# Kernel optimization log

Measured on AMD Instinct MI355X. Metric: run time of the kernel, lower is better.

The kernel has to match this reference:

```python
import jax, jax.numpy as jnp
import numpy as np

D_MODEL = 768
NHEAD = 12
HEAD_DIM = D_MODEL // NHEAD


def setup_inputs() -> dict:
    key = jax.random.key(0)
    ks = jax.random.split(key, 9)
    B, S = 1, 4096
    scale = 1.0 / np.sqrt(D_MODEL)
    x = jax.random.normal(ks[0], (B, S, D_MODEL), dtype=jnp.float32)
    # Linear params: weight [out,in] torch convention, bias [out]
    wq = jax.random.normal(ks[1], (D_MODEL, D_MODEL), dtype=jnp.float32) * scale
    bq = jnp.zeros((D_MODEL,), dtype=jnp.float32)
    wk = jax.random.normal(ks[2], (D_MODEL, D_MODEL), dtype=jnp.float32) * scale
    bk = jnp.zeros((D_MODEL,), dtype=jnp.float32)
    wv = jax.random.normal(ks[3], (D_MODEL, D_MODEL), dtype=jnp.float32) * scale
    bv = jnp.zeros((D_MODEL,), dtype=jnp.float32)
    wo = jax.random.normal(ks[4], (D_MODEL, D_MODEL), dtype=jnp.float32) * scale
    bo = jnp.zeros((D_MODEL,), dtype=jnp.float32)
    return {"x": x, "wq": wq, "bq": bq, "wk": wk, "bk": bk,
            "wv": wv, "bv": bv, "wo": wo, "bo": bo}


def reference(x, wq, bq, wk, bk, wv, bv, wo, bo):
    B, S, D = x.shape
    H, Hd = NHEAD, HEAD_DIM
    # projections (torch Linear: x @ W^T + b)
    q = (x @ wq.T + bq).reshape(B, S, H, Hd).transpose(0, 2, 1, 3)  # [B,H,S,Hd]
    k = (x @ wk.T + bk).reshape(B, S, H, Hd).transpose(0, 2, 1, 3)
    v = (x @ wv.T + bv).reshape(B, S, H, Hd).transpose(0, 2, 1, 3)
    scores = jnp.einsum('bhsd,bhtd->bhst', q, k) / jnp.sqrt(jnp.float32(Hd))  # [B,H,S,S]
    probs = jax.nn.softmax(scores, axis=-1)
    attn = jnp.einsum('bhst,bhtd->bhsd', probs, v)  # [B,H,S,Hd]
    attn = attn.transpose(0, 2, 1, 3).reshape(B, S, D)
    return attn @ wo.T + bo
```

## Files before the change

### kernel.cpp

```cpp
#include <hip/hip_runtime.h>
#include <hip/hip_bf16.h>

typedef __attribute__((ext_vector_type(8))) __bf16 bf16x8;
typedef __attribute__((ext_vector_type(4))) __bf16 bf16x4;
typedef __attribute__((ext_vector_type(4))) float f32x4;
typedef __attribute__((ext_vector_type(16))) float f32x16;
typedef __attribute__((ext_vector_type(2))) unsigned u32x2;

#define D_MODEL 768
#define SEQ     4096
#define NH      12
#define HD      64

#define QSCALE (0.125f * 1.44269504088896f)

__device__ __forceinline__ void gload_lds16(const void* g, void* l) {
    __builtin_amdgcn_global_load_lds(
        (const __attribute__((address_space(1))) void*)g,
        (__attribute__((address_space(3))) void*)l, 16, 0, 0);
}

__device__ __forceinline__ u32x2 plswap(unsigned a, unsigned b) {
    return __builtin_amdgcn_permlane32_swap(a, b, false, false);
}

__global__ __launch_bounds__(256) void cvt_kernel(
    const float* __restrict__ x,  const float* __restrict__ wq,
    const float* __restrict__ wk, const float* __restrict__ wv,
    const float* __restrict__ wo,
    __bf16* __restrict__ xb,  __bf16* __restrict__ wqb,
    __bf16* __restrict__ wkb, __bf16* __restrict__ wvb,
    __bf16* __restrict__ wob)
{
    const int XV = SEQ * D_MODEL / 4;
    const int WV = D_MODEL * D_MODEL / 4;
    const int total = XV + 4 * WV;
    for (int i = blockIdx.x * blockDim.x + threadIdx.x; i < total;
         i += gridDim.x * blockDim.x) {
        const float* src; __bf16* dst; int j;
        if      (i < XV)          { src = x;  dst = xb;  j = i; }
        else if (i < XV + WV)     { src = wq; dst = wqb; j = i - XV; }
        else if (i < XV + 2*WV)   { src = wk; dst = wkb; j = i - XV - WV; }
        else if (i < XV + 3*WV)   { src = wv; dst = wvb; j = i - XV - 2*WV; }
        else                      { src = wo; dst = wob; j = i - XV - 3*WV; }
        float4 v = ((const float4*)src)[j];
        bf16x4 o;
        o[0] = (__bf16)v.x; o[1] = (__bf16)v.y;
        o[2] = (__bf16)v.z; o[3] = (__bf16)v.w;
        ((bf16x4*)dst)[j] = o;
    }
}

__device__ __forceinline__ void gemm128_core(
    const __bf16* __restrict__ A, const __bf16* __restrict__ B, int KD,
    f32x4 acc[4][4], __bf16 (*As)[64], __bf16 (*Bs)[64])
{
    const int t = threadIdx.x;
    const int lane = t & 63, wid = t >> 6;
    const int wm = (wid & 1) * 64, wn = (wid >> 1) * 64;
    const int lr = lane & 15, lc = lane >> 4;
    const int rl = lane >> 3;
    const int cs = (lane & 7) ^ rl;

    const __bf16* ag = A + (size_t)(wid * 32 + rl) * KD + cs * 8;
    const __bf16* bg = B + (size_t)(wid * 32 + rl) * KD + cs * 8;

    for (int kt = 0; kt < KD / 64; ++kt) {
        __syncthreads();
        #pragma unroll
        for (int i = 0; i < 4; ++i) {
            gload_lds16(ag + (size_t)i * 8 * KD + kt * 64,
                        &As[wid * 32 + i * 8][0]);
            gload_lds16(bg + (size_t)i * 8 * KD + kt * 64,
                        &Bs[wid * 32 + i * 8][0]);
        }
        __syncthreads();

        #pragma unroll
        for (int kh = 0; kh < 2; ++kh) {
            bf16x8 af[4], bfr[4];
            #pragma unroll
            for (int mi = 0; mi < 4; ++mi)
                af[mi] = *(const bf16x8*)
                    &As[wm + mi * 16 + lr][(((kh << 2) | lc) ^ (lr & 7)) * 8];
            #pragma unroll
            for (int ni = 0; ni < 4; ++ni)
                bfr[ni] = *(const bf16x8*)
                    &Bs[wn + ni * 16 + lr][(((kh << 2) | lc) ^ (lr & 7)) * 8];
            __builtin_amdgcn_s_setprio(1);
            #pragma unroll
            for (int mi = 0; mi < 4; ++mi)
                #pragma unroll
                for (int ni = 0; ni < 4; ++ni)
                    acc[mi][ni] = __builtin_amdgcn_mfma_f32_16x16x32_bf16(
                        af[mi], bfr[ni], acc[mi][ni], 0, 0, 0);
            __builtin_amdgcn_s_setprio(0);
        }
    }
}

__global__ __launch_bounds__(256) void qkv_gemm(
    const __bf16* __restrict__ xb,
    const __bf16* __restrict__ wqb, const __bf16* __restrict__ wkb,
    const __bf16* __restrict__ wvb,
    const float* __restrict__ bq, const float* __restrict__ bk,
    const float* __restrict__ bv,
    __bf16* __restrict__ Qo, __bf16* __restrict__ Ko,
    __bf16* __restrict__ Vto)
{
    __shared__ __bf16 As[128][64];
    __shared__ __bf16 Bs[128][64];
    const int bm = blockIdx.x;
    const int seg = blockIdx.y / 6, bn = blockIdx.y % 6;
    const __bf16* B  = (seg == 0) ? wqb : (seg == 1) ? wkb : wvb;
    const float* bias = (seg == 0) ? bq : (seg == 1) ? bk : bv;

    f32x4 acc[4][4] = {};
    gemm128_core(xb + (size_t)bm * 128 * D_MODEL,
                 B  + (size_t)bn * 128 * D_MODEL, D_MODEL, acc, As, Bs);

    const int t = threadIdx.x, lane = t & 63, wid = t >> 6;
    const int wm = (wid & 1) * 64, wn = (wid >> 1) * 64;
    const int lr = lane & 15, lc = lane >> 4;
    const int m0 = bm * 128 + wm, n0 = bn * 128 + wn;

    if (seg < 2) {
        __bf16* O = (seg == 0) ? Qo : Ko;
        const float sc = (seg == 0) ? QSCALE : 1.0f;
        #pragma unroll
        for (int mi = 0; mi < 4; ++mi)
            #pragma unroll
            for (int ni = 0; ni < 4; ++ni) {
                int col = n0 + ni * 16 + lr;
                float bb = bias[col];
                #pragma unroll
                for (int r = 0; r < 4; ++r)
                    O[(size_t)(m0 + mi * 16 + lc * 4 + r) * D_MODEL + col] =
                        (__bf16)((acc[mi][ni][r] + bb) * sc);
            }
    } else {
        #pragma unroll
        for (int mi = 0; mi < 4; ++mi)
            #pragma unroll
            for (int ni = 0; ni < 4; ++ni) {
                int col = n0 + ni * 16 + lr;
                float bb = bias[col];
                bf16x4 pk;
                #pragma unroll
                for (int r = 0; r < 4; ++r)
                    pk[r] = (__bf16)(acc[mi][ni][r] + bb);
                *(bf16x4*)&Vto[(size_t)col * SEQ + m0 + mi * 16 + lc * 4] = pk;
            }
    }
}

__global__ __launch_bounds__(256) void attn_kernel(
    const __bf16* __restrict__ Q, const __bf16* __restrict__ K,
    const __bf16* __restrict__ Vt, __bf16* __restrict__ Attn)
{
    __shared__ __align__(16) char LDSc[32768];
    __bf16 (*Ks)[32][64] = (__bf16(*)[32][64])(LDSc);
    __bf16 (*Vs)[64][32] = (__bf16(*)[64][32])(LDSc + 16384);
    float* Mg = (float*)LDSc;
    float* Ml = (float*)(LDSc + 16384);

    const int bid = blockIdx.x;
    const int swz = (bid & 7) * 96 + (bid >> 3);
    const int h  = swz >> 6;
    const int q0 = (swz & 63) * 64;

    const int t = threadIdx.x, lane = t & 63, wid = t >> 6;
    const int qs = wid & 1, half = wid >> 1;
    const int ql = lane & 31, hi = lane >> 5;
    const int s7 = ql & 7;
    const int v2s = (ql >> 1) & 3;

    const int krl = lane >> 3, kcs = (lane & 7) ^ (lane >> 3);
    const int vrl = lane >> 2, vcs = (lane & 3) ^ ((lane >> 3) & 3);
    const __bf16* kg = K +
        (size_t)(half * 2048 + qs * 16 + krl) * D_MODEL + h * HD + kcs * 8;
    const __bf16* vg = Vt +
        (size_t)(h * HD + qs * 32 + vrl) * SEQ + half * 2048 + vcs * 8;

    const __bf16* qrow = Q + (size_t)(q0 + qs * 32 + ql) * D_MODEL + h * HD;
    bf16x8 qf[4];
    #pragma unroll
    for (int k4 = 0; k4 < 4; ++k4)
        qf[k4] = *(const bf16x8*)&qrow[k4 * 16 + hi * 8];

    f32x16 acc0 = {}, acc1 = {};
    float m_r = -1e30f, l_r = 0.f;

    gload_lds16(kg,                    &Ks[half * 2][qs * 16][0]);
    gload_lds16(kg + 8 * D_MODEL,      &Ks[half * 2][qs * 16 + 8][0]);
    gload_lds16(vg,                    &Vs[half * 2][qs * 32][0]);
    gload_lds16(vg + (size_t)16 * SEQ, &Vs[half * 2][qs * 32 + 16][0]);

    const int NT = 2048 / 32;

#define ATILE(CUR, PT, DOPF) do {                                             \
    __syncthreads();                                                          \
    if (DOPF) {                                                               \
        const __bf16* kgt = kg + (size_t)(PT) * 32 * D_MODEL;                 \
        const __bf16* vgt = vg + (PT) * 32;                                   \
        gload_lds16(kgt,               &Ks[half*2 + ((CUR)^1)][qs*16][0]);    \
        gload_lds16(kgt + 8*D_MODEL,   &Ks[half*2 + ((CUR)^1)][qs*16+8][0]);  \
        gload_lds16(vgt,               &Vs[half*2 + ((CUR)^1)][qs*32][0]);    \
        gload_lds16(vgt + (size_t)16*SEQ,                                     \
                    &Vs[half*2 + ((CUR)^1)][qs*32+16][0]);                    \
    }                                                                         \
    f32x16 st = {};                                                           \
    __builtin_amdgcn_s_setprio(1);                                            \
    _Pragma("unroll")                                                         \
    for (int k4 = 0; k4 < 4; ++k4) {                                          \
        bf16x8 kf = *(const bf16x8*)                                          \
            &Ks[half*2 + (CUR)][ql][((k4*2 + hi) ^ s7) * 8];                  \
        st = __builtin_amdgcn_mfma_f32_32x32x16_bf16(kf, qf[k4], st, 0,0,0);  \
    }                                                                         \
    __builtin_amdgcn_s_setprio(0);                                            \
    float mx = -1e30f;                                                        \
    _Pragma("unroll")                                                         \
    for (int r = 0; r < 16; ++r) mx = fmaxf(mx, st[r]);                       \
    {                                                                         \
        u32x2 mp = plswap(__float_as_uint(mx), __float_as_uint(mx));          \
        mx = fmaxf(__uint_as_float(mp[0]), __uint_as_float(mp[1]));           \
    }                                                                         \
    const bool skip = (bool)__all(mx - m_r <= 8.0f);                          \
    float mnew = skip ? m_r : fmaxf(m_r, mx);                                 \
    float corr = skip ? 1.0f : exp2f(m_r - mnew);                             \
    float rs = 0.f;                                                           \
    _Pragma("unroll")                                                         \
    for (int r = 0; r < 16; ++r) { st[r] = exp2f(st[r] - mnew); rs += st[r]; }\
    {                                                                         \
        u32x2 rp = plswap(__float_as_uint(rs), __float_as_uint(rs));          \
        rs = __uint_as_float(rp[0]) + __uint_as_float(rp[1]);                 \
    }                                                                         \
    l_r = l_r * corr + rs;  m_r = mnew;                                       \
    if (!skip) {                                                              \
        _Pragma("unroll")                                                     \
        for (int r = 0; r < 16; ++r) { acc0[r] *= corr; acc1[r] *= corr; }    \
    }                                                                         \
                                             \
    unsigned wA[4], wB[4];                                                    \
    _Pragma("unroll")                                                         \
    for (int g = 0; g < 4; ++g) {                                             \
        union { __bf16 h2[2]; unsigned u; } pa, pb;                           \
        pa.h2[0] = (__bf16)st[4*g + 0]; pa.h2[1] = (__bf16)st[4*g + 1];       \
        pb.h2[0] = (__bf16)st[4*g + 2]; pb.h2[1] = (__bf16)st[4*g + 3];       \
        wA[g] = pa.u; wB[g] = pb.u;                                           \
    }                                                                         \
    __builtin_amdgcn_s_setprio(1);                                            \
    _Pragma("unroll")                                                         \
    for (int kb = 0; kb < 2; ++kb) {                                          \
        u32x2 sA = plswap(wA[2*kb], wA[2*kb + 1]);                            \
        u32x2 sB = plswap(wB[2*kb], wB[2*kb + 1]);                            \
        union { unsigned u[4]; bf16x8 v; } fb;                                \
        fb.u[0] = sA[0]; fb.u[1] = sB[0]; fb.u[2] = sA[1]; fb.u[3] = sB[1];   \
        bf16x8 vf0 = *(const bf16x8*)                                         \
            &Vs[half*2 + (CUR)][ql][((kb*2 + hi) ^ v2s) * 8];                 \
        bf16x8 vf1 = *(const bf16x8*)                                         \
            &Vs[half*2 + (CUR)][32 + ql][((kb*2 + hi) ^ v2s) * 8];            \
        acc0 = __builtin_amdgcn_mfma_f32_32x32x16_bf16(vf0, fb.v, acc0,0,0,0);\
        acc1 = __builtin_amdgcn_mfma_f32_32x32x16_bf16(vf1, fb.v, acc1,0,0,0);\
    }                                                                         \
    __builtin_amdgcn_s_setprio(0);                                            \
} while (0)

    for (int kk = 0; kk < NT; kk += 2) {
        ATILE(0, kk + 1, 1);
        ATILE(1, kk + 2, (kk + 2 < NT));
    }
#undef ATILE

    __syncthreads();
    if (half == 1) {
        float* mybuf = Mg + qs * 2048 + lane * 32;
        #pragma unroll
        for (int j = 0; j < 4; ++j) {
            f32x4 v; v[0]=acc0[4*j]; v[1]=acc0[4*j+1]; v[2]=acc0[4*j+2]; v[3]=acc0[4*j+3];
            *(f32x4*)&mybuf[(j ^ s7) * 4] = v;
        }
        #pragma unroll
        for (int j = 0; j < 4; ++j) {
            f32x4 v; v[0]=acc1[4*j]; v[1]=acc1[4*j+1]; v[2]=acc1[4*j+2]; v[3]=acc1[4*j+3];
            *(f32x4*)&mybuf[((4 + j) ^ s7) * 4] = v;
        }
        Ml[(qs * 2 + 0) * 64 + lane] = m_r;
        Ml[(qs * 2 + 1) * 64 + lane] = l_r;
    }
    __syncthreads();
    if (half == 0) {
        float m1 = Ml[(qs * 2 + 0) * 64 + lane];
        float l1 = Ml[(qs * 2 + 1) * 64 + lane];
        float mstar = fmaxf(m_r, m1);
        float s0 = exp2f(m_r - mstar), s1 = exp2f(m1 - mstar);
        float li = 1.0f / (l_r * s0 + l1 * s1);
        const float* obuf = Mg + qs * 2048 + lane * 32;

        __bf16* orow = Attn + (size_t)(q0 + qs * 32 + ql) * D_MODEL
                       + h * HD + hi * 4;
        #pragma unroll
        for (int g = 0; g < 4; ++g) {
            f32x4 a1 = *(const f32x4*)&obuf[(g ^ s7) * 4];
            union { __bf16 h4[4]; uint2 v2; } w;
            #pragma unroll
            for (int i = 0; i < 4; ++i)
                w.h4[i] = (__bf16)((acc0[4*g+i] * s0 + a1[i] * s1) * li);
            *(uint2*)&orow[g * 8] = w.v2;

            f32x4 b1 = *(const f32x4*)&obuf[((4 + g) ^ s7) * 4];
            #pragma unroll
            for (int i = 0; i < 4; ++i)
                w.h4[i] = (__bf16)((acc1[4*g+i] * s0 + b1[i] * s1) * li);
            *(uint2*)&orow[32 + g * 8] = w.v2;
        }
    }
}

__global__ __launch_bounds__(256) void out_gemm(
    const __bf16* __restrict__ Ab, const __bf16* __restrict__ wob,
    const float* __restrict__ bo, float* __restrict__ out)
{
    __shared__ __bf16 As[128][64];
    __shared__ __bf16 Bs[128][64];
    const int bm = blockIdx.x, bn = blockIdx.y;
    f32x4 acc[4][4] = {};
    gemm128_core(Ab  + (size_t)bm * 128 * D_MODEL,
                 wob + (size_t)bn * 128 * D_MODEL, D_MODEL, acc, As, Bs);

    const int t = threadIdx.x, lane = t & 63, wid = t >> 6;
    const int wm = (wid & 1) * 64, wn = (wid >> 1) * 64;
    const int lr = lane & 15, lc = lane >> 4;
    const int m0 = bm * 128 + wm, n0 = bn * 128 + wn;
    #pragma unroll
    for (int mi = 0; mi < 4; ++mi)
        #pragma unroll
        for (int ni = 0; ni < 4; ++ni) {
            int col = n0 + ni * 16 + lr;
            float bb = bo[col];
            #pragma unroll
            for (int r = 0; r < 4; ++r)
                out[(size_t)(m0 + mi * 16 + lc * 4 + r) * D_MODEL + col] =
                    acc[mi][ni][r] + bb;
        }
}

extern "C" void kernel_launch(void* const* d_in, const int* in_sizes, int n_in,
                              void* d_out, int out_size, void* d_ws, size_t ws_size,
                              hipStream_t stream) {
    const float* x  = (const float*)d_in[0];
    const float* wq = (const float*)d_in[1];
    const float* bq = (const float*)d_in[2];
    const float* wk = (const float*)d_in[3];
    const float* bk = (const float*)d_in[4];
    const float* wv = (const float*)d_in[5];
    const float* bv = (const float*)d_in[6];
    const float* wo = (const float*)d_in[7];
    const float* bo = (const float*)d_in[8];

    char* ws = (char*)d_ws;
    const size_t XB_SZ = (size_t)SEQ * D_MODEL * 2;
    const size_t W_SZ  = (size_t)D_MODEL * D_MODEL * 2;
    __bf16* xb  = (__bf16*)(ws);
    __bf16* wqb = (__bf16*)(ws + XB_SZ);
    __bf16* wkb = (__bf16*)(ws + XB_SZ + W_SZ);
    __bf16* wvb = (__bf16*)(ws + XB_SZ + 2 * W_SZ);
    __bf16* wob = (__bf16*)(ws + XB_SZ + 3 * W_SZ);
    __bf16* Qb  = (__bf16*)(ws + XB_SZ + 4 * W_SZ);
    __bf16* Kb  = (__bf16*)(ws + 2 * XB_SZ + 4 * W_SZ);
    __bf16* Vtb = (__bf16*)(ws + 3 * XB_SZ + 4 * W_SZ);
    __bf16* Ab  = (__bf16*)(ws + 4 * XB_SZ + 4 * W_SZ);

    cvt_kernel<<<1024, 256, 0, stream>>>(x, wq, wk, wv, wo,
                                         xb, wqb, wkb, wvb, wob);
    qkv_gemm<<<dim3(32, 18), 256, 0, stream>>>(xb, wqb, wkb, wvb,
                                               bq, bk, bv, Qb, Kb, Vtb);
    attn_kernel<<<768, 256, 0, stream>>>(Qb, Kb, Vtb, Ab);
    out_gemm<<<dim3(32, 6), 256, 0, stream>>>(Ab, wob, bo, (float*)d_out);
}
```

Before: 162.9 us.

## Split attention KV range four ways per block with per-wave private LDS pipelines

Each block now handles 32 queries instead of 64, with each of the four waves processing a quarter of the key sequence through its own double-buffered K/V LDS region. This removes the per-tile __syncthreads in favour of per-wave vmcnt waits, and doubles the grid to 1536 blocks. A four-way softmax merge at the end combines the partial outputs. Tree reductions replace the serial max and sum chains. In exchange, LDS per block doubles to 64KB, which may lower occupancy, and each K/V tile is now loaded once per 32 queries instead of once per 64.

```diff
diff --git a/kernel.cpp b/kernel.cpp
--- a/kernel.cpp
+++ b/kernel.cpp
@@ -158,31 +158,28 @@
     const __bf16* __restrict__ Q, const __bf16* __restrict__ K,
     const __bf16* __restrict__ Vt, __bf16* __restrict__ Attn)
 {
-    __shared__ __align__(16) char LDSc[32768];
-    __bf16 (*Ks)[32][64] = (__bf16(*)[32][64])(LDSc);
-    __bf16 (*Vs)[64][32] = (__bf16(*)[64][32])(LDSc + 16384);
-    float* Mg = (float*)LDSc;
-    float* Ml = (float*)(LDSc + 16384);
+    __shared__ __align__(16) char LDSc[65536];
+    __bf16 (*Ks)[2][32][64] = (__bf16(*)[2][32][64])(LDSc);
+    __bf16 (*Vs)[2][64][32] = (__bf16(*)[2][64][32])(LDSc + 32768);
 
     const int bid = blockIdx.x;
-    const int swz = (bid & 7) * 96 + (bid >> 3);
-    const int h  = swz >> 6;
-    const int q0 = (swz & 63) * 64;
+    const int swz = (bid & 7) * 192 + (bid >> 3);
+    const int h  = swz >> 7;
+    const int q0 = (swz & 127) * 32;
 
     const int t = threadIdx.x, lane = t & 63, wid = t >> 6;
-    const int qs = wid & 1, half = wid >> 1;
     const int ql = lane & 31, hi = lane >> 5;
     const int s7 = ql & 7;
     const int v2s = (ql >> 1) & 3;
 
-    const int krl = lane >> 3, kcs = (lane & 7) ^ (lane >> 3);
-    const int vrl = lane >> 2, vcs = (lane & 3) ^ ((lane >> 3) & 3);
+    const int kcs = (lane & 7) ^ (lane >> 3);
+    const int vcs = (lane & 3) ^ ((lane >> 3) & 3);
     const __bf16* kg = K +
-        (size_t)(half * 2048 + qs * 16 + krl) * D_MODEL + h * HD + kcs * 8;
+        (size_t)(wid * 1024 + (lane >> 3)) * D_MODEL + h * HD + kcs * 8;
     const __bf16* vg = Vt +
-        (size_t)(h * HD + qs * 32 + vrl) * SEQ + half * 2048 + vcs * 8;
-
-    const __bf16* qrow = Q + (size_t)(q0 + qs * 32 + ql) * D_MODEL + h * HD;
+        (size_t)(h * HD + (lane >> 2)) * SEQ + wid * 1024 + vcs * 8;
+
+    const __bf16* qrow = Q + (size_t)(q0 + ql) * D_MODEL + h * HD;
     bf16x8 qf[4];
     #pragma unroll
     for (int k4 = 0; k4 < 4; ++k4)
@@ -191,36 +188,42 @@
     f32x16 acc0 = {}, acc1 = {};
     float m_r = -1e30f, l_r = 0.f;
 
-    gload_lds16(kg,                    &Ks[half * 2][qs * 16][0]);
-    gload_lds16(kg + 8 * D_MODEL,      &Ks[half * 2][qs * 16 + 8][0]);
-    gload_lds16(vg,                    &Vs[half * 2][qs * 32][0]);
-    gload_lds16(vg + (size_t)16 * SEQ, &Vs[half * 2][qs * 32 + 16][0]);
-
-    const int NT = 2048 / 32;
+    #define STAGE(BUF, TT) do {                                               \
+        const __bf16* kgt = kg + (size_t)(TT) * 32 * D_MODEL;                 \
+        const __bf16* vgt = vg + (TT) * 32;                                   \
+        _Pragma("unroll")                                                     \
+        for (int i = 0; i < 4; ++i)                                           \
+            gload_lds16(kgt + (size_t)i * 8 * D_MODEL, &Ks[wid][BUF][i*8][0]);\
+        _Pragma("unroll")                                                     \
+        for (int i = 0; i < 4; ++i)                                           \
+            gload_lds16(vgt + (size_t)i * 16 * SEQ, &Vs[wid][BUF][i*16][0]);  \
+    } while (0)
+
+    STAGE(0, 0);
 
 #define ATILE(CUR, PT, DOPF) do {                                             \
-    __syncthreads();                                                          \
     if (DOPF) {                                                               \
-        const __bf16* kgt = kg + (size_t)(PT) * 32 * D_MODEL;                 \
-        const __bf16* vgt = vg + (PT) * 32;                                   \
-        gload_lds16(kgt,               &Ks[half*2 + ((CUR)^1)][qs*16][0]);    \
-        gload_lds16(kgt + 8*D_MODEL,   &Ks[half*2 + ((CUR)^1)][qs*16+8][0]);  \
-        gload_lds16(vgt,               &Vs[half*2 + ((CUR)^1)][qs*32][0]);    \
-        gload_lds16(vgt + (size_t)16*SEQ,                                     \
-                    &Vs[half*2 + ((CUR)^1)][qs*32+16][0]);                    \
+        STAGE((CUR) ^ 1, PT);                                                 \
+        asm volatile("s_waitcnt vmcnt(8)" ::: "memory");                      \
+    } else {                                                                  \
+        asm volatile("s_waitcnt vmcnt(0)" ::: "memory");                      \
     }                                                                         \
     f32x16 st = {};                                                           \
     __builtin_amdgcn_s_setprio(1);                                            \
     _Pragma("unroll")                                                         \
     for (int k4 = 0; k4 < 4; ++k4) {                                          \
         bf16x8 kf = *(const bf16x8*)                                          \
-            &Ks[half*2 + (CUR)][ql][((k4*2 + hi) ^ s7) * 8];                  \
+            &Ks[wid][CUR][ql][((k4*2 + hi) ^ s7) * 8];                        \
         st = __builtin_amdgcn_mfma_f32_32x32x16_bf16(kf, qf[k4], st, 0,0,0);  \
     }                                                                         \
     __builtin_amdgcn_s_setprio(0);                                            \
-    float mx = -1e30f;                                                        \
-    _Pragma("unroll")                                                         \
-    for (int r = 0; r < 16; ++r) mx = fmaxf(mx, st[r]);                       \
+                                                                \
+    float t8[8];                                                              \
+    _Pragma("unroll")                                                         \
+    for (int i = 0; i < 8; ++i) t8[i] = fmaxf(st[i], st[i + 8]);              \
+    _Pragma("unroll")                                                         \
+    for (int i = 0; i < 4; ++i) t8[i] = fmaxf(t8[i], t8[i + 4]);              \
+    float mx = fmaxf(fmaxf(t8[0], t8[1]), fmaxf(t8[2], t8[3]));               \
     {                                                                         \
         u32x2 mp = plswap(__float_as_uint(mx), __float_as_uint(mx));          \
         mx = fmaxf(__uint_as_float(mp[0]), __uint_as_float(mp[1]));           \
@@ -228,9 +231,15 @@
     const bool skip = (bool)__all(mx - m_r <= 8.0f);                          \
     float mnew = skip ? m_r : fmaxf(m_r, mx);                                 \
     float corr = skip ? 1.0f : exp2f(m_r - mnew);                             \
-    float rs = 0.f;                                                           \
-    _Pragma("unroll")                                                         \
-    for (int r = 0; r < 16; ++r) { st[r] = exp2f(st[r] - mnew); rs += st[r]; }\
+    _Pragma("unroll")                                                         \
+    for (int r = 0; r < 16; ++r) st[r] = exp2f(st[r] - mnew);                 \
+                                                                \
+    float u8[8];                                                              \
+    _Pragma("unroll")                                                         \
+    for (int i = 0; i < 8; ++i) u8[i] = st[i] + st[i + 8];                    \
+    _Pragma("unroll")                                                         \
+    for (int i = 0; i < 4; ++i) u8[i] += u8[i + 4];                           \
+    float rs = (u8[0] + u8[1]) + (u8[2] + u8[3]);                             \
     {                                                                         \
         u32x2 rp = plswap(__float_as_uint(rs), __float_as_uint(rs));          \
         rs = __uint_as_float(rp[0]) + __uint_as_float(rp[1]);                 \
@@ -240,7 +249,7 @@
         _Pragma("unroll")                                                     \
         for (int r = 0; r < 16; ++r) { acc0[r] *= corr; acc1[r] *= corr; }    \
     }                                                                         \
-                                             \
+                                               \
     unsigned wA[4], wB[4];                                                    \
     _Pragma("unroll")                                                         \
     for (int g = 0; g < 4; ++g) {                                             \
@@ -257,61 +266,75 @@
         union { unsigned u[4]; bf16x8 v; } fb;                                \
         fb.u[0] = sA[0]; fb.u[1] = sB[0]; fb.u[2] = sA[1]; fb.u[3] = sB[1];   \
         bf16x8 vf0 = *(const bf16x8*)                                         \
-            &Vs[half*2 + (CUR)][ql][((kb*2 + hi) ^ v2s) * 8];                 \
+            &Vs[wid][CUR][ql][((kb*2 + hi) ^ v2s) * 8];                       \
         bf16x8 vf1 = *(const bf16x8*)                                         \
-            &Vs[half*2 + (CUR)][32 + ql][((kb*2 + hi) ^ v2s) * 8];            \
+            &Vs[wid][CUR][32 + ql][((kb*2 + hi) ^ v2s) * 8];                  \
         acc0 = __builtin_amdgcn_mfma_f32_32x32x16_bf16(vf0, fb.v, acc0,0,0,0);\
         acc1 = __builtin_amdgcn_mfma_f32_32x32x16_bf16(vf1, fb.v, acc1,0,0,0);\
     }                                                                         \
     __builtin_amdgcn_s_setprio(0);                                            \
 } while (0)
 
+    const int NT = 32;
     for (int kk = 0; kk < NT; kk += 2) {
         ATILE(0, kk + 1, 1);
         ATILE(1, kk + 2, (kk + 2 < NT));
     }
 #undef ATILE
-
-    __syncthreads();
-    if (half == 1) {
-        float* mybuf = Mg + qs * 2048 + lane * 32;
+#undef STAGE
+
+    if (wid != 0) {
+        float* myM = (float*)&Ks[wid][0][0][0];
         #pragma unroll
         for (int j = 0; j < 4; ++j) {
             f32x4 v; v[0]=acc0[4*j]; v[1]=acc0[4*j+1]; v[2]=acc0[4*j+2]; v[3]=acc0[4*j+3];
-            *(f32x4*)&mybuf[(j ^ s7) * 4] = v;
+            *(f32x4*)&myM[lane * 32 + ((j ^ s7) * 4)] = v;
         }
         #pragma unroll
         for (int j = 0; j < 4; ++j) {
             f32x4 v; v[0]=acc1[4*j]; v[1]=acc1[4*j+1]; v[2]=acc1[4*j+2]; v[3]=acc1[4*j+3];
-            *(f32x4*)&mybuf[((4 + j) ^ s7) * 4] = v;
-        }
-        Ml[(qs * 2 + 0) * 64 + lane] = m_r;
-        Ml[(qs * 2 + 1) * 64 + lane] = l_r;
+            *(f32x4*)&myM[lane * 32 + (((4 + j) ^ s7) * 4)] = v;
+        }
+        float* myl = (float*)&Vs[wid][0][0][0];
+        myl[lane] = m_r;
+        myl[64 + lane] = l_r;
     }
     __syncthreads();
-    if (half == 0) {
-        float m1 = Ml[(qs * 2 + 0) * 64 + lane];
-        float l1 = Ml[(qs * 2 + 1) * 64 + lane];
-        float mstar = fmaxf(m_r, m1);
-        float s0 = exp2f(m_r - mstar), s1 = exp2f(m1 - mstar);
-        float li = 1.0f / (l_r * s0 + l1 * s1);
-        const float* obuf = Mg + qs * 2048 + lane * 32;
-
-        __bf16* orow = Attn + (size_t)(q0 + qs * 32 + ql) * D_MODEL
-                       + h * HD + hi * 4;
+    if (wid == 0) {
+        float mM = m_r, lL = l_r;
+        #pragma unroll
+        for (int w = 1; w < 4; ++w) {
+            const float* Mw = (const float*)&Ks[w][0][0][0];
+            const float* lw = (const float*)&Vs[w][0][0][0];
+            float m1 = lw[lane], l1 = lw[64 + lane];
+            float mstar = fmaxf(mM, m1);
+            float sc0 = exp2f(mM - mstar), sc1 = exp2f(m1 - mstar);
+            #pragma unroll
+            for (int j = 0; j < 4; ++j) {
+                f32x4 a1 = *(const f32x4*)&Mw[lane * 32 + ((j ^ s7) * 4)];
+                #pragma unroll
+                for (int i = 0; i < 4; ++i)
+                    acc0[4*j + i] = acc0[4*j + i] * sc0 + a1[i] * sc1;
+                f32x4 b1 = *(const f32x4*)&Mw[lane * 32 + (((4 + j) ^ s7) * 4)];
+                #pragma unroll
+                for (int i = 0; i < 4; ++i)
+                    acc1[4*j + i] = acc1[4*j + i] * sc0 + b1[i] * sc1;
+            }
+            lL = lL * sc0 + l1 * sc1;
+            mM = mstar;
+        }
+        float li = 1.0f / lL;
+        __bf16* orow = Attn + (size_t)(q0 + ql) * D_MODEL + h * HD + hi * 4;
         #pragma unroll
         for (int g = 0; g < 4; ++g) {
-            f32x4 a1 = *(const f32x4*)&obuf[(g ^ s7) * 4];
             union { __bf16 h4[4]; uint2 v2; } w;
             #pragma unroll
             for (int i = 0; i < 4; ++i)
-                w.h4[i] = (__bf16)((acc0[4*g+i] * s0 + a1[i] * s1) * li);
+                w.h4[i] = (__bf16)(acc0[4*g + i] * li);
             *(uint2*)&orow[g * 8] = w.v2;
-
-            f32x4 b1 = *(const f32x4*)&obuf[((4 + g) ^ s7) * 4];
             #pragma unroll
             for (int i = 0; i < 4; ++i)
-                w.h4[i] = (__bf16)((acc1[4*g+i] * s0 + b1[i] * s1) * li);
+                w.h4[i] = (__bf16)(acc1[4*g + i] * li);
             *(uint2*)&orow[32 + g * 8] = w.v2;
         }
     }
@@ -375,6 +398,6 @@
                                          xb, wqb, wkb, wvb, wob);
     qkv_gemm<<<dim3(32, 18), 256, 0, stream>>>(xb, wqb, wkb, wvb,
                                                bq, bk, bv, Qb, Kb, Vtb);
-    attn_kernel<<<768, 256, 0, stream>>>(Qb, Kb, Vtb, Ab);
+    attn_kernel<<<1536, 256, 0, stream>>>(Qb, Kb, Vtb, Ab);
     out_gemm<<<dim3(32, 6), 256, 0, stream>>>(Ab, wob, bo, (float*)d_out);
 }
```

After: 178.8 us. +9.8%, slower.
